# Kernel tuning notes

Measured on AMD Instinct MI355X. Metric: run time of the kernel, lower is better.

## Reference

```python
import jax, jax.numpy as jnp
import numpy as np

N_NODES = 50000
N_EDGES = 800000
D = 64
L = 2
EPS = 1e-9


def setup_inputs() -> dict:
    key = jax.random.key(0)
    ks = jax.random.split(key, 8)
    node_feats = jax.random.normal(ks[0], (N_NODES, D), dtype=jnp.float32)
    edge_src = jax.random.randint(ks[1], (N_EDGES,), 0, N_NODES, dtype=jnp.int32)
    edge_dst = jnp.sort(jax.random.randint(ks[2], (N_EDGES,), 0, N_NODES, dtype=jnp.int32))
    edge_w = jax.random.uniform(ks[3], (N_EDGES,), dtype=jnp.float32)
    W0 = jax.random.normal(ks[4], (D, D), dtype=jnp.float32) / np.sqrt(D)
    b0 = jax.random.normal(ks[5], (D,), dtype=jnp.float32) * 0.02
    W1 = jax.random.normal(ks[6], (D, D), dtype=jnp.float32) / np.sqrt(D)
    b1 = jax.random.normal(ks[7], (D,), dtype=jnp.float32) * 0.02
    return {"node_feats": node_feats, "edge_src": edge_src, "edge_dst": edge_dst,
            "edge_w": edge_w, "W0": W0, "b0": b0, "W1": W1, "b1": b1}


def reference(node_feats, edge_src, edge_dst, edge_w, W0, b0, W1, b1):
    n = node_feats.shape[0]
    # per-destination normalizer: sum of incoming edge weights + eps
    denom = jax.ops.segment_sum(edge_w, edge_dst, num_segments=n) + EPS  # [N]
    feats = node_feats
    for _ in range(L):
        # gather neighbor feats, weight, scatter-add to destination, normalize
        weighted = edge_w[:, None] * feats[edge_src]                      # [E, D]
        msg = jax.ops.segment_sum(weighted, edge_dst, num_segments=n)     # [N, D]
        msg = msg / denom[:, None]
        feats = jax.nn.relu(feats @ W0.T + b0 + msg @ W1.T + b1)
        # isolated nodes: segment_sum gives 0 -> msg = 0, matching msg=0.0 in torch
    return feats
```

## Files before the change

### kernel.cpp

```cpp
#include <hip/hip_runtime.h>

#define D 64
#define EPSV 1e-9f

typedef __attribute__((ext_vector_type(8))) short bf8_t;
typedef __attribute__((ext_vector_type(4))) float f4_t;

__device__ inline float bf2f(short u) {
    union { unsigned int i; float f; } v;
    v.i = ((unsigned int)(unsigned short)u) << 16;
    return v.f;
}
__device__ inline unsigned short f2bf(float f) {
    union { float f; unsigned int i; } v; v.f = f;
    unsigned int r = v.i + 0x7fff + ((v.i >> 16) & 1);
    return (unsigned short)(r >> 16);
}

__global__ void prep_kernel(const float* __restrict__ node_feats,
                            const int*   __restrict__ edge_dst,
                            const float* __restrict__ W0,
                            const float* __restrict__ W1,
                            int* __restrict__ row_off,
                            unsigned short* __restrict__ Wpack,
                            unsigned short* __restrict__ X,
                            int n_nodes, int n_edges, int cvtb)
{
    const int bid = blockIdx.x;
    const int tid = threadIdx.x;
    if (bid < cvtb) {
        const int i = bid * 256 + tid;
        if (i < n_nodes * 16) {
            const float4 v = ((const float4*)node_feats)[i];
            const int row = i >> 4, c4 = (i & 15) * 4;
            unsigned short* p = X + row * 128 + c4;
            p[0] = f2bf(v.x); p[1] = f2bf(v.y); p[2] = f2bf(v.z); p[3] = f2bf(v.w);
        }
    } else if (bid < cvtb + 32) {
        const int idx = (bid - cvtb) * 256 + tid;
        const int j = idx & 7, lane = (idx >> 3) & 63, kk = (idx >> 9) & 3, t = idx >> 11;
        const int k = kk * 32 + (lane >> 4) * 8 + j;
        const int d = t * 16 + (lane & 15);
        const float v = (k < D) ? W0[d * D + k] : W1[d * D + (k - D)];
        Wpack[idx] = f2bf(v);
    } else {
        const int n = (bid - cvtb - 32) * 256 + tid;
        if (n <= n_nodes) {
            int lo = 0, hi = n_edges;
            while (lo < hi) {
                const int mid = (lo + hi) >> 1;
                if (edge_dst[mid] < n) lo = mid + 1; else hi = mid;
            }
            row_off[n] = lo;
        }
    }
}

__global__ __launch_bounds__(256, 6) void aggregate_kernel(
    unsigned short* __restrict__ X,
    const int*   __restrict__ row_off,
    const int*   __restrict__ edge_src,
    const float* __restrict__ edge_w,
    int n_nodes)
{
    const int lane = threadIdx.x & 63;
    const int wib  = threadIdx.x >> 6;
    int nA = blockIdx.x * 8 + wib * 2;
    int nB = nA + 1;
    if (nA >= n_nodes) nA = n_nodes - 1;
    if (nB >= n_nodes) nB = n_nodes - 1;
    nA = __builtin_amdgcn_readfirstlane(nA);
    nB = __builtin_amdgcn_readfirstlane(nB);

    const int sA = row_off[nA], eA = row_off[nA + 1];
    const int sB = row_off[nB], eB = row_off[nB + 1];
    const int dA = eA - sA, dB = eB - sB;
    const int dmax = dA > dB ? dA : dB;

    const int slot = lane >> 3;
    const int fo   = (lane & 7) * 8;

    float aA[8], aB[8];
    #pragma unroll
    for (int m = 0; m < 8; ++m) { aA[m] = 0.f; aB[m] = 0.f; }
    float wsA = 0.f, wsB = 0.f;

    for (int base = 0; base < dmax; base += 16) {
        const int  ejA0 = sA + base + slot,  ejA1 = ejA0 + 8;
        const int  ejB0 = sB + base + slot,  ejB1 = ejB0 + 8;
        const bool vA0 = ejA0 < eA, vA1 = ejA1 < eA;
        const bool vB0 = ejB0 < eB, vB1 = ejB1 < eB;
        const float wA0 = vA0 ? edge_w[ejA0] : 0.f;
        const float wA1 = vA1 ? edge_w[ejA1] : 0.f;
        const float wB0 = vB0 ? edge_w[ejB0] : 0.f;
        const float wB1 = vB1 ? edge_w[ejB1] : 0.f;
        const int srcA0 = vA0 ? edge_src[ejA0] : 0;
        const int srcA1 = vA1 ? edge_src[ejA1] : 0;
        const int srcB0 = vB0 ? edge_src[ejB0] : 0;
        const int srcB1 = vB1 ? edge_src[ejB1] : 0;
        const bf8_t fA0 = *(const bf8_t*)(X + srcA0 * 128 + fo);
        const bf8_t fA1 = *(const bf8_t*)(X + srcA1 * 128 + fo);
        const bf8_t fB0 = *(const bf8_t*)(X + srcB0 * 128 + fo);
        const bf8_t fB1 = *(const bf8_t*)(X + srcB1 * 128 + fo);
        #pragma unroll
        for (int m = 0; m < 8; ++m) {
            aA[m] = fmaf(wA0, bf2f(fA0[m]), fmaf(wA1, bf2f(fA1[m]), aA[m]));
            aB[m] = fmaf(wB0, bf2f(fB0[m]), fmaf(wB1, bf2f(fB1[m]), aB[m]));
        }
        wsA += wA0 + wA1;
        wsB += wB0 + wB1;
    }

    #pragma unroll
    for (int off = 8; off <= 32; off <<= 1) {
        #pragma unroll
        for (int m = 0; m < 8; ++m) {
            aA[m] += __shfl_xor(aA[m], off);
            aB[m] += __shfl_xor(aB[m], off);
        }
        wsA += __shfl_xor(wsA, off);
        wsB += __shfl_xor(wsB, off);
    }

    const float invA = 1.0f / (wsA + EPSV);
    const float invB = 1.0f / (wsB + EPSV);
    if (lane < 8) {
        bf8_t mv;
        #pragma unroll
        for (int m = 0; m < 8; ++m) mv[m] = (short)f2bf(aA[m] * invA);
        *(bf8_t*)(X + nA * 128 + 64 + fo) = mv;
    } else if (lane < 16) {
        bf8_t mv;
        #pragma unroll
        for (int m = 0; m < 8; ++m) mv[m] = (short)f2bf(aB[m] * invB);
        *(bf8_t*)(X + nB * 128 + 64 + fo) = mv;
    }
}

template<int OUT_F32>
__global__ __launch_bounds__(256, 4) void gemm_mfma(
    const unsigned short* __restrict__ X,
    const unsigned short* __restrict__ Wpack,
    const float* __restrict__ b0,
    const float* __restrict__ b1,
    void* __restrict__ outp,
    int ntiles, int waves_total)
{
    const int lane = threadIdx.x & 63;
    const int wib  = threadIdx.x >> 6;
    const int wave = __builtin_amdgcn_readfirstlane(blockIdx.x * 4 + wib);

    bf8_t bf[4][4];
    #pragma unroll
    for (int t = 0; t < 4; ++t)
        #pragma unroll
        for (int kk = 0; kk < 4; ++kk)
            bf[t][kk] = *(const bf8_t*)(Wpack + ((t * 4 + kk) * 64 + lane) * 8);

    float bias[4];
    #pragma unroll
    for (int t = 0; t < 4; ++t) {
        const int col = t * 16 + (lane & 15);
        bias[t] = b0[col] + b1[col];
    }

    for (int tile = wave; tile < ntiles; tile += waves_total) {
        const int rowbase = tile * 16;
        const int arow = rowbase + (lane & 15);
        const unsigned short* ap = X + arow * 128 + (lane >> 4) * 8;

        bf8_t af[4];
        #pragma unroll
        for (int kk = 0; kk < 4; ++kk) af[kk] = *(const bf8_t*)(ap + kk * 32);

        f4_t acc[4];
        #pragma unroll
        for (int t = 0; t < 4; ++t) acc[t] = (f4_t){0.f, 0.f, 0.f, 0.f};

        #pragma unroll
        for (int t = 0; t < 4; ++t)
            #pragma unroll
            for (int kk = 0; kk < 4; ++kk)
                acc[t] = __builtin_amdgcn_mfma_f32_16x16x32_bf16(af[kk], bf[t][kk], acc[t], 0, 0, 0);

        #pragma unroll
        for (int t = 0; t < 4; ++t) {
            #pragma unroll
            for (int r = 0; r < 4; ++r) {
                const float v = fmaxf(acc[t][r] + bias[t], 0.0f);
                const int row = rowbase + (lane >> 4) * 4 + r;
                const int col = t * 16 + (lane & 15);
                if (OUT_F32) ((float*)outp)[row * 64 + col] = v;
                else ((unsigned short*)outp)[row * 128 + col] = f2bf(v);
            }
        }
    }
}

extern "C" void kernel_launch(void* const* d_in, const int* in_sizes, int n_in,
                              void* d_out, int out_size, void* d_ws, size_t ws_size,
                              hipStream_t stream) {
    const float* node_feats = (const float*)d_in[0];
    const int*   edge_src   = (const int*)  d_in[1];
    const int*   edge_dst   = (const int*)  d_in[2];
    const float* edge_w     = (const float*)d_in[3];
    const float* W0         = (const float*)d_in[4];
    const float* b0         = (const float*)d_in[5];
    const float* W1         = (const float*)d_in[6];
    const float* b1         = (const float*)d_in[7];

    const int n_nodes = in_sizes[0] / D;
    const int n_edges = in_sizes[1];

    char* ws = (char*)d_ws;
    int*            row_off = (int*)ws;
    unsigned short* Wpack   = (unsigned short*)(ws + 204800);
    unsigned short* X0      = (unsigned short*)(ws + 237568);
    unsigned short* X1      = (unsigned short*)d_out;

    const int cvtb = (n_nodes * 16 + 255) / 256;
    const int offb = (n_nodes + 1 + 255) / 256;
    prep_kernel<<<cvtb + 32 + offb, 256, 0, stream>>>(node_feats, edge_dst, W0, W1,
                                                      row_off, Wpack, X0,
                                                      n_nodes, n_edges, cvtb);

    const int agrid  = (n_nodes + 7) / 8;
    const int ntiles = (n_nodes + 15) / 16;
    const int ggrid  = 256;
    const int gwaves = ggrid * 4;

    aggregate_kernel<<<agrid, 256, 0, stream>>>(X0, row_off, edge_src, edge_w, n_nodes);
    gemm_mfma<0><<<ggrid, 256, 0, stream>>>(X0, Wpack, b0, b1, X1, ntiles, gwaves);
    aggregate_kernel<<<agrid, 256, 0, stream>>>(X1, row_off, edge_src, edge_w, n_nodes);
    gemm_mfma<1><<<ggrid, 256, 0, stream>>>(X1, Wpack, b0, b1, d_out, ntiles, gwaves);
}
```

Measured before the change: 73.42 us.

## Fuse neighbor aggregation and MFMA GEMM into one per-layer kernel

```diff
diff --git a/kernel.cpp b/kernel.cpp
--- a/kernel.cpp
+++ b/kernel.cpp
@@ -33,7 +33,7 @@
         if (i < n_nodes * 16) {
             const float4 v = ((const float4*)node_feats)[i];
             const int row = i >> 4, c4 = (i & 15) * 4;
-            unsigned short* p = X + row * 128 + c4;
+            unsigned short* p = X + row * 64 + c4;
             p[0] = f2bf(v.x); p[1] = f2bf(v.y); p[2] = f2bf(v.z); p[3] = f2bf(v.w);
         }
     } else if (bid < cvtb + 32) {
@@ -56,143 +56,120 @@
     }
 }
 
-__global__ __launch_bounds__(256, 6) void aggregate_kernel(
-    unsigned short* __restrict__ X,
+template<int OUT_F32>
+__global__ __launch_bounds__(256, 4) void layer_kernel(
+    const unsigned short* __restrict__ Xin,
     const int*   __restrict__ row_off,
     const int*   __restrict__ edge_src,
     const float* __restrict__ edge_w,
-    int n_nodes)
-{
-    const int lane = threadIdx.x & 63;
-    const int wib  = threadIdx.x >> 6;
-    int nA = blockIdx.x * 8 + wib * 2;
-    int nB = nA + 1;
-    if (nA >= n_nodes) nA = n_nodes - 1;
-    if (nB >= n_nodes) nB = n_nodes - 1;
-    nA = __builtin_amdgcn_readfirstlane(nA);
-    nB = __builtin_amdgcn_readfirstlane(nB);
-
-    const int sA = row_off[nA], eA = row_off[nA + 1];
-    const int sB = row_off[nB], eB = row_off[nB + 1];
-    const int dA = eA - sA, dB = eB - sB;
-    const int dmax = dA > dB ? dA : dB;
-
-    const int slot = lane >> 3;
-    const int fo   = (lane & 7) * 8;
-
-    float aA[8], aB[8];
-    #pragma unroll
-    for (int m = 0; m < 8; ++m) { aA[m] = 0.f; aB[m] = 0.f; }
-    float wsA = 0.f, wsB = 0.f;
-
-    for (int base = 0; base < dmax; base += 16) {
-        const int  ejA0 = sA + base + slot,  ejA1 = ejA0 + 8;
-        const int  ejB0 = sB + base + slot,  ejB1 = ejB0 + 8;
-        const bool vA0 = ejA0 < eA, vA1 = ejA1 < eA;
-        const bool vB0 = ejB0 < eB, vB1 = ejB1 < eB;
-        const float wA0 = vA0 ? edge_w[ejA0] : 0.f;
-        const float wA1 = vA1 ? edge_w[ejA1] : 0.f;
-        const float wB0 = vB0 ? edge_w[ejB0] : 0.f;
-        const float wB1 = vB1 ? edge_w[ejB1] : 0.f;
-        const int srcA0 = vA0 ? edge_src[ejA0] : 0;
-        const int srcA1 = vA1 ? edge_src[ejA1] : 0;
-        const int srcB0 = vB0 ? edge_src[ejB0] : 0;
-        const int srcB1 = vB1 ? edge_src[ejB1] : 0;
-        const bf8_t fA0 = *(const bf8_t*)(X + srcA0 * 128 + fo);
-        const bf8_t fA1 = *(const bf8_t*)(X + srcA1 * 128 + fo);
-        const bf8_t fB0 = *(const bf8_t*)(X + srcB0 * 128 + fo);
-        const bf8_t fB1 = *(const bf8_t*)(X + srcB1 * 128 + fo);
-        #pragma unroll
-        for (int m = 0; m < 8; ++m) {
-            aA[m] = fmaf(wA0, bf2f(fA0[m]), fmaf(wA1, bf2f(fA1[m]), aA[m]));
-            aB[m] = fmaf(wB0, bf2f(fB0[m]), fmaf(wB1, bf2f(fB1[m]), aB[m]));
-        }
-        wsA += wA0 + wA1;
-        wsB += wB0 + wB1;
-    }
-
-    #pragma unroll
-    for (int off = 8; off <= 32; off <<= 1) {
-        #pragma unroll
-        for (int m = 0; m < 8; ++m) {
-            aA[m] += __shfl_xor(aA[m], off);
-            aB[m] += __shfl_xor(aB[m], off);
-        }
-        wsA += __shfl_xor(wsA, off);
-        wsB += __shfl_xor(wsB, off);
-    }
-
-    const float invA = 1.0f / (wsA + EPSV);
-    const float invB = 1.0f / (wsB + EPSV);
-    if (lane < 8) {
-        bf8_t mv;
-        #pragma unroll
-        for (int m = 0; m < 8; ++m) mv[m] = (short)f2bf(aA[m] * invA);
-        *(bf8_t*)(X + nA * 128 + 64 + fo) = mv;
-    } else if (lane < 16) {
-        bf8_t mv;
-        #pragma unroll
-        for (int m = 0; m < 8; ++m) mv[m] = (short)f2bf(aB[m] * invB);
-        *(bf8_t*)(X + nB * 128 + 64 + fo) = mv;
-    }
-}
-
-template<int OUT_F32>
-__global__ __launch_bounds__(256, 4) void gemm_mfma(
-    const unsigned short* __restrict__ X,
     const unsigned short* __restrict__ Wpack,
     const float* __restrict__ b0,
     const float* __restrict__ b1,
     void* __restrict__ outp,
-    int ntiles, int waves_total)
+    int n_nodes)
 {
+    __shared__ __align__(16) unsigned short lds_msg[16][72];
+
     const int lane = threadIdx.x & 63;
-    const int wib  = threadIdx.x >> 6;
-    const int wave = __builtin_amdgcn_readfirstlane(blockIdx.x * 4 + wib);
-
-    bf8_t bf[4][4];
-    #pragma unroll
-    for (int t = 0; t < 4; ++t)
+    const int w    = threadIdx.x >> 6;
+    const int rowbase = blockIdx.x * 16;
+
+    const int nb = rowbase + w * 4;
+    int s[4], e[4];
+    #pragma unroll
+    for (int i = 0; i < 4; ++i) {
+        int n = nb + i; if (n >= n_nodes) n = n_nodes - 1;
+        s[i] = row_off[n]; e[i] = row_off[n + 1];
+    }
+    int dmax = 0;
+    #pragma unroll
+    for (int i = 0; i < 4; ++i) { const int d = e[i] - s[i]; if (d > dmax) dmax = d; }
+
+    const int slot = lane >> 3;
+    const int fo   = (lane & 7) * 8;
+
+    float acc[4][8];
+    float ws[4];
+    #pragma unroll
+    for (int i = 0; i < 4; ++i) {
+        ws[i] = 0.f;
         #pragma unroll
-        for (int kk = 0; kk < 4; ++kk)
-            bf[t][kk] = *(const bf8_t*)(Wpack + ((t * 4 + kk) * 64 + lane) * 8);
-
-    float bias[4];
-    #pragma unroll
-    for (int t = 0; t < 4; ++t) {
-        const int col = t * 16 + (lane & 15);
-        bias[t] = b0[col] + b1[col];
-    }
-
-    for (int tile = wave; tile < ntiles; tile += waves_total) {
-        const int rowbase = tile * 16;
-        const int arow = rowbase + (lane & 15);
-        const unsigned short* ap = X + arow * 128 + (lane >> 4) * 8;
-
-        bf8_t af[4];
+        for (int m = 0; m < 8; ++m) acc[i][m] = 0.f;
+    }
+
+    for (int base = 0; base < dmax; base += 16) {
         #pragma unroll
-        for (int kk = 0; kk < 4; ++kk) af[kk] = *(const bf8_t*)(ap + kk * 32);
-
-        f4_t acc[4];
+        for (int i = 0; i < 4; ++i) {
+            const int  ej0 = s[i] + base + slot;
+            const int  ej1 = ej0 + 8;
+            const bool v0 = ej0 < e[i], v1 = ej1 < e[i];
+            const float w0 = v0 ? edge_w[ej0] : 0.f;
+            const float w1 = v1 ? edge_w[ej1] : 0.f;
+            const int  sc0 = v0 ? edge_src[ej0] : 0;
+            const int  sc1 = v1 ? edge_src[ej1] : 0;
+            const bf8_t f0 = *(const bf8_t*)(Xin + sc0 * 64 + fo);
+            const bf8_t f1 = *(const bf8_t*)(Xin + sc1 * 64 + fo);
+            #pragma unroll
+            for (int m = 0; m < 8; ++m)
+                acc[i][m] = fmaf(w0, bf2f(f0[m]), fmaf(w1, bf2f(f1[m]), acc[i][m]));
+            ws[i] += w0 + w1;
+        }
+    }
+
+    #pragma unroll
+    for (int off = 8; off <= 32; off <<= 1) {
         #pragma unroll
-        for (int t = 0; t < 4; ++t) acc[t] = (f4_t){0.f, 0.f, 0.f, 0.f};
-
-        #pragma unroll
-        for (int t = 0; t < 4; ++t)
+        for (int i = 0; i < 4; ++i) {
             #pragma unroll
-            for (int kk = 0; kk < 4; ++kk)
-                acc[t] = __builtin_amdgcn_mfma_f32_16x16x32_bf16(af[kk], bf[t][kk], acc[t], 0, 0, 0);
-
-        #pragma unroll
-        for (int t = 0; t < 4; ++t) {
+            for (int m = 0; m < 8; ++m) acc[i][m] += __shfl_xor(acc[i][m], off);
+            ws[i] += __shfl_xor(ws[i], off);
+        }
+    }
+
+    const int g = lane >> 3;
+    #pragma unroll
+    for (int i = 0; i < 4; ++i) {
+        if (g == i) {
+            const float inv = 1.0f / (ws[i] + EPSV);
+            bf8_t mv;
             #pragma unroll
-            for (int r = 0; r < 4; ++r) {
-                const float v = fmaxf(acc[t][r] + bias[t], 0.0f);
-                const int row = rowbase + (lane >> 4) * 4 + r;
-                const int col = t * 16 + (lane & 15);
-                if (OUT_F32) ((float*)outp)[row * 64 + col] = v;
-                else ((unsigned short*)outp)[row * 128 + col] = f2bf(v);
-            }
+            for (int m = 0; m < 8; ++m) mv[m] = (short)f2bf(acc[i][m] * inv);
+            *(bf8_t*)(&lds_msg[w * 4 + i][fo]) = mv;
+        }
+    }
+
+    __syncthreads();
+
+    bf8_t bfr[4];
+    #pragma unroll
+    for (int kk = 0; kk < 4; ++kk)
+        bfr[kk] = *(const bf8_t*)(Wpack + ((w * 4 + kk) * 64 + lane) * 8);
+
+    const int arow16 = lane & 15;
+    const int koff   = (lane >> 4) * 8;
+    int arow = rowbase + arow16; if (arow >= n_nodes) arow = n_nodes - 1;
+    const unsigned short* ap = Xin + arow * 64 + koff;
+
+    bf8_t af[4];
+    af[0] = *(const bf8_t*)(ap);
+    af[1] = *(const bf8_t*)(ap + 32);
+    af[2] = *(const bf8_t*)(&lds_msg[arow16][koff]);
+    af[3] = *(const bf8_t*)(&lds_msg[arow16][koff + 32]);
+
+    f4_t acc4 = (f4_t){0.f, 0.f, 0.f, 0.f};
+    #pragma unroll
+    for (int kk = 0; kk < 4; ++kk)
+        acc4 = __builtin_amdgcn_mfma_f32_16x16x32_bf16(af[kk], bfr[kk], acc4, 0, 0, 0);
+
+    const int col  = w * 16 + (lane & 15);
+    const float bias = b0[col] + b1[col];
+    #pragma unroll
+    for (int r = 0; r < 4; ++r) {
+        const int row = rowbase + (lane >> 4) * 4 + r;
+        if (row < n_nodes) {
+            const float v = fmaxf(acc4[r] + bias, 0.0f);
+            if (OUT_F32) ((float*)outp)[row * 64 + col] = v;
+            else ((unsigned short*)outp)[row * 64 + col] = f2bf(v);
         }
     }
 }
@@ -216,7 +193,7 @@
     int*            row_off = (int*)ws;
     unsigned short* Wpack   = (unsigned short*)(ws + 204800);
     unsigned short* X0      = (unsigned short*)(ws + 237568);
-    unsigned short* X1      = (unsigned short*)d_out;
+    unsigned short* X1      = (unsigned short*)(ws + 237568 + 6400000);
 
     const int cvtb = (n_nodes * 16 + 255) / 256;
     const int offb = (n_nodes + 1 + 255) / 256;
@@ -224,13 +201,10 @@
                                                       row_off, Wpack, X0,
                                                       n_nodes, n_edges, cvtb);
 
-    const int agrid  = (n_nodes + 7) / 8;
     const int ntiles = (n_nodes + 15) / 16;
-    const int ggrid  = 256;
-    const int gwaves = ggrid * 4;
-
-    aggregate_kernel<<<agrid, 256, 0, stream>>>(X0, row_off, edge_src, edge_w, n_nodes);
-    gemm_mfma<0><<<ggrid, 256, 0, stream>>>(X0, Wpack, b0, b1, X1, ntiles, gwaves);
-    aggregate_kernel<<<agrid, 256, 0, stream>>>(X1, row_off, edge_src, edge_w, n_nodes);
-    gemm_mfma<1><<<ggrid, 256, 0, stream>>>(X1, Wpack, b0, b1, d_out, ntiles, gwaves);
-}
+
+    layer_kernel<0><<<ntiles, 256, 0, stream>>>(X0, row_off, edge_src, edge_w,
+                                                Wpack, b0, b1, X1, n_nodes);
+    layer_kernel<1><<<ntiles, 256, 0, stream>>>(X1, row_off, edge_src, edge_w,
+                                                Wpack, b0, b1, d_out, n_nodes);
+}
```

After: 75.49 us. 1.03x slower.
